# Kernel tuning notes

Measured on AMD Instinct MI355X. Metric: run time of the kernel, lower is better.

Reference implementation:

```python
import jax, jax.numpy as jnp
import numpy as np

ATOM_DIMS = [119, 9, 11, 12, 9, 5, 8, 2, 2]   # torch_geometric smiles x_map cardinalities
EDGE_DIMS = [22, 6, 2]                          # e_map cardinalities
N_NODES = 100_000
N_EDGES = 1_600_000
N_GRAPHS = 1024
HID = 64
MLP_HID = 128
N_LAYERS = 3
BN_EPS = 1e-5


def setup_inputs() -> dict:
    key = jax.random.key(0)
    ks = iter(jax.random.split(key, 64))

    # integer inputs (per-column in-range categorical indices)
    x = jnp.stack([jax.random.randint(next(ks), (N_NODES,), 0, d) for d in ATOM_DIMS], axis=1).astype(jnp.int32)
    edge_attr = jnp.stack([jax.random.randint(next(ks), (N_EDGES,), 0, d) for d in EDGE_DIMS], axis=1).astype(jnp.int32)
    edge_index = jax.random.randint(next(ks), (2, N_EDGES), 0, N_NODES).astype(jnp.int32)
    batch = jnp.sort(jax.random.randint(next(ks), (N_NODES,), 0, N_GRAPHS)).astype(jnp.int32)

    def emb(k, shape, scale=0.1):
        return jax.random.normal(k, shape, dtype=jnp.float32) * scale

    # atom embedding tables, padded to max cardinality and stacked: [9, 119, HID]
    atom_emb = emb(next(ks), (len(ATOM_DIMS), max(ATOM_DIMS), HID))
    # per-layer edge embedding tables: [L, 3, 22, HID]
    edge_emb = emb(next(ks), (N_LAYERS, len(EDGE_DIMS), max(EDGE_DIMS), HID))

    lin1_w = emb(next(ks), (N_LAYERS, MLP_HID, HID))
    lin1_b = emb(next(ks), (N_LAYERS, MLP_HID))
    bn_gamma = 1.0 + emb(next(ks), (N_LAYERS, MLP_HID))
    bn_beta = emb(next(ks), (N_LAYERS, MLP_HID))
    bn_mean = emb(next(ks), (N_LAYERS, MLP_HID))
    bn_var = jax.random.uniform(next(ks), (N_LAYERS, MLP_HID), dtype=jnp.float32, minval=0.5, maxval=1.5)
    lin2_w = emb(next(ks), (N_LAYERS, HID, MLP_HID))
    lin2_b = emb(next(ks), (N_LAYERS, HID))
    eps = jnp.zeros((N_LAYERS,), dtype=jnp.float32)

    return dict(x=x, edge_index=edge_index, edge_attr=edge_attr, batch=batch,
                atom_emb=atom_emb, edge_emb=edge_emb,
                lin1_w=lin1_w, lin1_b=lin1_b, bn_gamma=bn_gamma, bn_beta=bn_beta,
                bn_mean=bn_mean, bn_var=bn_var, lin2_w=lin2_w, lin2_b=lin2_b, eps=eps)


def _feature_embed(tables, idx):
    # tables: [F, V, D], idx: [N, F] -> sum_f tables[f][idx[:, f]] : [N, D]
    return jax.vmap(lambda t, i: t[i], in_axes=(0, 1))(tables, idx).sum(axis=0)


def reference(x, edge_index, edge_attr, batch, atom_emb, edge_emb,
              lin1_w, lin1_b, bn_gamma, bn_beta, bn_mean, bn_var,
              lin2_w, lin2_b, eps):
    n_nodes = x.shape[0]
    src, dst = edge_index[0], edge_index[1]

    h = _feature_embed(atom_emb, x)  # [N, HID]
    pooled = [jax.ops.segment_sum(h, batch, num_segments=N_GRAPHS)]

    for l in range(N_LAYERS):
        e = _feature_embed(edge_emb[l], edge_attr)           # [E, HID]
        msg = jax.nn.relu(h[src] + e)                         # gather + edge embed + relu
        agg = jax.ops.segment_sum(msg, dst, num_segments=n_nodes)  # scatter-add
        z = jax.nn.relu((1.0 + eps[l]) * h + agg)
        # NodeMLP: lin1 -> BatchNorm1d (eval, running stats) -> relu -> lin2
        z = z @ lin1_w[l].T + lin1_b[l]
        z = (z - bn_mean[l]) * jax.lax.rsqrt(bn_var[l] + BN_EPS) * bn_gamma[l] + bn_beta[l]
        z = jax.nn.relu(z)
        h = z @ lin2_w[l].T + lin2_b[l]
        h = jax.nn.relu(h)  # outer relu in GIN.forward (dropout is no-op in eval)
        pooled.append(jax.ops.segment_sum(h, batch, num_segments=N_GRAPHS))

    return jnp.concatenate(pooled, axis=1)  # [G, HID*(L+1)] = [1024, 256]
```

## Files before the change

### kernel.cpp

```cpp
#include <hip/hip_runtime.h>

#define N_NODES 100000
#define N_EDGES 1600000
#define N_GRAPHS 1024
#define HID 64
#define MLP_HID 128
#define N_COMBO 264
#define NBUCK 98
#define BCAP 20480
#define CHUNK 6144

#define NB_EMBED 1563
#define NPREP (3*N_COMBO*HID + 3*MLP_HID*HID + 3*MLP_HID)
#define NB_PREP 296

typedef __attribute__((ext_vector_type(8))) short bf16x8;
typedef __attribute__((ext_vector_type(4))) float f32x4;
typedef __attribute__((ext_vector_type(2))) float f32x2;

static __device__ __forceinline__ float bf2f(unsigned short u) {
    union { unsigned int i; float f; } v; v.i = ((unsigned int)u) << 16; return v.f;
}
static __device__ __forceinline__ unsigned short f2bf(float f) {
    union { float f; unsigned int i; } v; v.f = f;
    unsigned int u = v.i;
    unsigned int r = u + 0x7FFFu + ((u >> 16) & 1u);
    return (unsigned short)(r >> 16);
}
static __device__ __forceinline__ f32x2 bfpair(unsigned int u) {
    union { unsigned int i; float f; } lo, hi;
    lo.i = u << 16;
    hi.i = u & 0xFFFF0000u;
    f32x2 r; r.x = lo.f; r.y = hi.f; return r;
}
static __device__ __forceinline__ unsigned int pack2bf(float a, float b) {
    return (unsigned int)f2bf(a) | ((unsigned int)f2bf(b) << 16);
}

__global__ __launch_bounds__(256) void misc_kernel(
    const int* __restrict__ x, const float* __restrict__ atom_emb,
    const int* __restrict__ batch, unsigned short* __restrict__ h,
    float* __restrict__ out,
    const float* __restrict__ edge_emb,
    const float* __restrict__ w1, const float* __restrict__ w2,
    const float* __restrict__ b1, const float* __restrict__ bn_g,
    const float* __restrict__ bn_b, const float* __restrict__ bn_m,
    const float* __restrict__ bn_v,
    float* __restrict__ comb,
    unsigned short* __restrict__ w1b, unsigned short* __restrict__ w2b,
    float* __restrict__ alpha, float* __restrict__ beta)
{
    const int bid = blockIdx.x;
    const int tid = threadIdx.x;

    if (bid < NB_EMBED) {
        int f = tid & 63;
        int q = __builtin_amdgcn_readfirstlane(tid >> 6);
        int base = bid * 64 + q * 16;
        float run = 0.f;
        int cg = -1;
        for (int k = 0; k < 16; ++k) {
            int gn = base + k;
            if (gn >= N_NODES) break;
            const int* xp = x + gn * 9;
            float acc = 0.f;
#pragma unroll
            for (int j = 0; j < 9; ++j) {
                int idx = xp[j];
                acc += atom_emb[(j * 119 + idx) * HID + f];
            }
            h[(size_t)gn * HID + f] = f2bf(acc);
            int g = batch[gn];
            if (g != cg) {
                if (cg >= 0) atomicAdd(&out[cg * 256 + f], run);
                run = 0.f; cg = g;
            }
            run += acc;
        }
        if (cg >= 0) atomicAdd(&out[cg * 256 + f], run);
    } else {
        int t = (bid - NB_EMBED) * 256 + tid;
        const int NC = 3 * N_COMBO * HID;
        const int NW = 3 * MLP_HID * HID;
        if (t < NC) {
            int d = t & 63;
            int c = (t >> 6) % N_COMBO;
            int l = (t >> 6) / N_COMBO;
            int a0 = c / 12, r = c % 12, a1 = r >> 1, a2 = r & 1;
            const float* base = edge_emb + (size_t)l * 3 * 22 * HID;
            comb[t] = base[(0 * 22 + a0) * HID + d]
                    + base[(1 * 22 + a1) * HID + d]
                    + base[(2 * 22 + a2) * HID + d];
        } else if (t < NC + NW) {
            int i = t - NC;
            w1b[i] = f2bf(w1[i]);
            w2b[i] = f2bf(w2[i]);
        } else if (t < NC + NW + 3 * MLP_HID) {
            int i = t - NC - NW;
            float a = rsqrtf(bn_v[i] + 1e-5f) * bn_g[i];
            alpha[i] = a;
            beta[i] = (b1[i] - bn_m[i]) * a + bn_b[i];
        }
    }
}

__global__ __launch_bounds__(256) void bscatter_kernel(
    const int* __restrict__ ei, const int* __restrict__ ea,
    int* __restrict__ bcur, unsigned long long* __restrict__ ebuf)
{
    __shared__ unsigned long long stage[CHUNK];
    __shared__ int hist[NBUCK];
    __shared__ int lbase[NBUCK];
    __shared__ int shift[NBUCK];
    __shared__ int sbuf[128];

    int tid = threadIdx.x;
    int base = blockIdx.x * CHUNK;
    int n_here = min(CHUNK, N_EDGES - base);

    for (int i = tid; i < NBUCK; i += 256) hist[i] = 0;
    __syncthreads();
    for (int i = tid; i < n_here; i += 256)
        atomicAdd(&hist[ei[N_EDGES + base + i] >> 10], 1);
    __syncthreads();
    if (tid < 128) sbuf[tid] = (tid < NBUCK) ? hist[tid] : 0;
    __syncthreads();
    for (int s = 1; s < 128; s <<= 1) {
        int u = 0;
        if (tid < 128 && tid >= s) u = sbuf[tid - s];
        __syncthreads();
        if (tid < 128) sbuf[tid] += u;
        __syncthreads();
    }
    if (tid < NBUCK) lbase[tid] = sbuf[tid] - hist[tid];
    __syncthreads();
    if (tid < NBUCK) {
        int c = hist[tid];
        if (c > 0) {
            int g = tid * BCAP + atomicAdd(&bcur[tid], c);
            shift[tid] = g - lbase[tid];
        }
        hist[tid] = lbase[tid];
    }
    __syncthreads();
    for (int i = tid; i < n_here; i += 256) {
        int e = base + i;
        int src = ei[e];
        int dst = ei[N_EDGES + e];
        int combo = (ea[e * 3 + 0] * 6 + ea[e * 3 + 1]) * 2 + ea[e * 3 + 2];
        int pos = atomicAdd(&hist[dst >> 10], 1);
        stage[pos] = (unsigned long long)(unsigned)(src | (combo << 17))
                   | ((unsigned long long)(unsigned)dst << 32);
    }
    __syncthreads();
    for (int i = tid; i < n_here; i += 256) {
        unsigned long long en = stage[i];
        ebuf[shift[(int)(en >> 32) >> 10] + i] = en;
    }
}

__global__ __launch_bounds__(256) void csr_build_kernel(
    const unsigned long long* __restrict__ ebuf, const int* __restrict__ bcur,
    int* __restrict__ cnt, int* __restrict__ off, int* __restrict__ csr_e)
{
    __shared__ int nh[1024];
    __shared__ int cur[1024];
    __shared__ int part[256];

    int b = blockIdx.x;
    int tid = threadIdx.x;
    int nodeBase = b << 10;
    int limit = min(1024, N_NODES - nodeBase);
    int beg = b * BCAP;
    int end = beg + bcur[b];

    for (int i = tid; i < 1024; i += 256) nh[i] = 0;
    __syncthreads();
    for (int i = beg + tid; i < end; i += 256)
        atomicAdd(&nh[(int)(ebuf[i] >> 32) - nodeBase], 1);
    __syncthreads();

    int s0 = nh[tid * 4], s1 = nh[tid * 4 + 1], s2 = nh[tid * 4 + 2], s3 = nh[tid * 4 + 3];
    part[tid] = s0 + s1 + s2 + s3;
    __syncthreads();
    for (int st = 1; st < 256; st <<= 1) {
        int v = 0;
        if (tid >= st) v = part[tid - st];
        __syncthreads();
        if (tid >= st) part[tid] += v;
        __syncthreads();
    }
    int e0 = (tid ? part[tid - 1] : 0);
    int e1 = e0 + s0, e2 = e1 + s1, e3 = e2 + s2;
    cur[tid * 4 + 0] = e0; cur[tid * 4 + 1] = e1;
    cur[tid * 4 + 2] = e2; cur[tid * 4 + 3] = e3;
    int excl[4] = {e0, e1, e2, e3};
    int cval[4] = {s0, s1, s2, s3};
#pragma unroll
    for (int j = 0; j < 4; ++j) {
        int nl = tid * 4 + j;
        if (nl < limit) {
            cnt[nodeBase + nl] = cval[j];
            off[nodeBase + nl] = beg + excl[j];
        }
    }
    __syncthreads();
    for (int i = beg + tid; i < end; i += 256) {
        unsigned long long en = ebuf[i];
        int pos = atomicAdd(&cur[(int)(en >> 32) - nodeBase], 1);
        csr_e[beg + pos] = (int)(unsigned)en;
    }
}

__global__ __launch_bounds__(256) void gather_kernel(
    const int* __restrict__ cnt, const int* __restrict__ off,
    const int* __restrict__ csr_e, const unsigned short* __restrict__ h,
    const float* __restrict__ comb_l, const float* __restrict__ eps_p,
    unsigned short* __restrict__ zbuf)
{
    const int tid = threadIdx.x;
    const int lane = tid & 63;
    const int grp = lane >> 3;
    const int fo = (lane & 7) << 3;
    const int n = blockIdx.x * 32 + (tid >> 6) * 8 + grp;

    const int beg = off[n];
    const int end = beg + cnt[n];

    const f32x2 zero2 = {0.f, 0.f};
    f32x2 a0 = zero2, a1 = zero2, a2 = zero2, a3 = zero2;

#define EDGE_ACC(PK)                                                               \
    {                                                                              \
        int pk_ = (PK);                                                            \
        uint4 hv = *reinterpret_cast<const uint4*>(h + (pk_ & 0x1FFFF) * HID + fo);\
        const float4* ep_ = reinterpret_cast<const float4*>(comb_l + (pk_ >> 17) * HID + fo); \
        float4 e0_ = ep_[0], e1_ = ep_[1];                                         \
        a0 += __builtin_elementwise_max(bfpair(hv.x) + (f32x2){e0_.x, e0_.y}, zero2); \
        a1 += __builtin_elementwise_max(bfpair(hv.y) + (f32x2){e0_.z, e0_.w}, zero2); \
        a2 += __builtin_elementwise_max(bfpair(hv.z) + (f32x2){e1_.x, e1_.y}, zero2); \
        a3 += __builtin_elementwise_max(bfpair(hv.w) + (f32x2){e1_.z, e1_.w}, zero2); \
    }

    int i = beg;
    for (; i + 1 < end; i += 2) {
        int pk0 = csr_e[i];
        int pk1 = csr_e[i + 1];
        EDGE_ACC(pk0);
        EDGE_ACC(pk1);
    }
    if (i < end) EDGE_ACC(csr_e[i]);
#undef EDGE_ACC

    uint4 hn = *reinterpret_cast<const uint4*>(h + (size_t)n * HID + fo);
    float ep1 = 1.0f + eps_p[0];
    f32x2 ep2 = {ep1, ep1};
    f32x2 z0 = __builtin_elementwise_max(ep2 * bfpair(hn.x) + a0, zero2);
    f32x2 z1 = __builtin_elementwise_max(ep2 * bfpair(hn.y) + a1, zero2);
    f32x2 z2 = __builtin_elementwise_max(ep2 * bfpair(hn.z) + a2, zero2);
    f32x2 z3 = __builtin_elementwise_max(ep2 * bfpair(hn.w) + a3, zero2);
    uint4 o;
    o.x = pack2bf(z0.x, z0.y);
    o.y = pack2bf(z1.x, z1.y);
    o.z = pack2bf(z2.x, z2.y);
    o.w = pack2bf(z3.x, z3.y);
    *reinterpret_cast<uint4*>(zbuf + (size_t)n * HID + fo) = o;
}

__global__ __launch_bounds__(256) void mlp_kernel(
    const unsigned short* __restrict__ zbuf, unsigned short* __restrict__ h,
    const unsigned short* __restrict__ w1b, const unsigned short* __restrict__ w2b,
    const float* __restrict__ alpha, const float* __restrict__ beta,
    const float* __restrict__ b2, const int* __restrict__ batch,
    float* __restrict__ out, int out_col, int write_h)
{
    __shared__ unsigned short us[128 * MLP_HID];
    __shared__ int sbatch[128];

    const int tid = threadIdx.x;
    const int lane = tid & 63;
    const int w = __builtin_amdgcn_readfirstlane(tid >> 6);
    const int base = blockIdx.x * 128;
    const int r16 = lane & 15;
    const int g4 = lane >> 4;

    if (tid < 128) sbatch[tid] = (base + tid < N_NODES) ? batch[base + tid] : -1;

    bf16x8 awf[2][2];
#pragma unroll
    for (int mo = 0; mo < 2; ++mo)
#pragma unroll
        for (int kt = 0; kt < 2; ++kt) {
            int o = (2 * w + mo) * 16 + r16;
            awf[mo][kt] = *reinterpret_cast<const bf16x8*>(w1b + o * HID + kt * 32 + g4 * 8);
        }
    float4 al[2], be[2];
#pragma unroll
    for (int mo = 0; mo < 2; ++mo) {
        int o0 = (2 * w + mo) * 16 + g4 * 4;
        al[mo] = *reinterpret_cast<const float4*>(alpha + o0);
        be[mo] = *reinterpret_cast<const float4*>(beta + o0);
    }

    char* usb = (char*)us;
#pragma unroll
    for (int nt = 0; nt < 8; ++nt) {
        bf16x8 zf[2];
#pragma unroll
        for (int kt = 0; kt < 2; ++kt)
            zf[kt] = *reinterpret_cast<const bf16x8*>(
                zbuf + (size_t)(base + nt * 16 + r16) * HID + kt * 32 + g4 * 8);
        f32x4 acc[2] = {(f32x4){0.f, 0.f, 0.f, 0.f}, (f32x4){0.f, 0.f, 0.f, 0.f}};
#pragma unroll
        for (int mo = 0; mo < 2; ++mo)
#pragma unroll
            for (int kt = 0; kt < 2; ++kt)
                acc[mo] = __builtin_amdgcn_mfma_f32_16x16x32_bf16(
                    awf[mo][kt], zf[kt], acc[mo], 0, 0, 0);
        int node = nt * 16 + r16;
#pragma unroll
        for (int mo = 0; mo < 2; ++mo) {
            int o0 = (2 * w + mo) * 16 + g4 * 4;
            f32x4 a = acc[mo];
            unsigned lo = pack2bf(fmaxf(a[0] * al[mo].x + be[mo].x, 0.f),
                                  fmaxf(a[1] * al[mo].y + be[mo].y, 0.f));
            unsigned hi = pack2bf(fmaxf(a[2] * al[mo].z + be[mo].z, 0.f),
                                  fmaxf(a[3] * al[mo].w + be[mo].w, 0.f));
            int byte = (node * 256 + o0 * 2) ^ ((node & 7) << 4);
            *reinterpret_cast<uint2*>(usb + byte) = make_uint2(lo, hi);
        }
    }
    __syncthreads();

    bf16x8 b2frag[4];
#pragma unroll
    for (int kt = 0; kt < 4; ++kt)
        b2frag[kt] = *reinterpret_cast<const bf16x8*>(
            w2b + (w * 16 + r16) * MLP_HID + kt * 32 + g4 * 8);

    const int o = w * 16 + r16;
    const float bias = b2[o];
    int gprev = -2;
    float run = 0.f;
#pragma unroll
    for (int mt = 0; mt < 8; ++mt) {
        f32x4 acc2 = (f32x4){0.f, 0.f, 0.f, 0.f};
#pragma unroll
        for (int kt = 0; kt < 4; ++kt) {
            int node = mt * 16 + r16;
            int byte = (node * 256 + (kt * 32 + g4 * 8) * 2) ^ ((node & 7) << 4);
            bf16x8 af = *reinterpret_cast<const bf16x8*>(usb + byte);
            acc2 = __builtin_amdgcn_mfma_f32_16x16x32_bf16(af, b2frag[kt], acc2, 0, 0, 0);
        }
#pragma unroll
        for (int r = 0; r < 4; ++r) {
            int node = mt * 16 + g4 * 4 + r;
            int gn = base + node;
            float v = fmaxf(acc2[r] + bias, 0.f);
            if (write_h && gn < N_NODES) h[(size_t)gn * HID + o] = f2bf(v);
            int gb = sbatch[node];
            if (gb != gprev) {
                if (gprev >= 0) atomicAdd(&out[gprev * 256 + out_col + o], run);
                run = 0.f;
                gprev = gb;
            }
            if (gb >= 0) run += v;
        }
    }
    if (gprev >= 0) atomicAdd(&out[gprev * 256 + out_col + o], run);
}

extern "C" void kernel_launch(void* const* d_in, const int* in_sizes, int n_in,
                              void* d_out, int out_size, void* d_ws, size_t ws_size,
                              hipStream_t stream)
{
    const int*   x        = (const int*)d_in[0];
    const int*   ei       = (const int*)d_in[1];
    const int*   ea       = (const int*)d_in[2];
    const int*   batch    = (const int*)d_in[3];
    const float* atom_emb = (const float*)d_in[4];
    const float* edge_emb = (const float*)d_in[5];
    const float* w1       = (const float*)d_in[6];
    const float* b1       = (const float*)d_in[7];
    const float* bn_g     = (const float*)d_in[8];
    const float* bn_b     = (const float*)d_in[9];
    const float* bn_m     = (const float*)d_in[10];
    const float* bn_v     = (const float*)d_in[11];
    const float* w2       = (const float*)d_in[12];
    const float* b2       = (const float*)d_in[13];
    const float* eps      = (const float*)d_in[14];

    float* out = (float*)d_out;

    const size_t NODE_PAD = 100096;
    char* ws = (char*)d_ws;
    unsigned short* h     = (unsigned short*)ws; ws += NODE_PAD * HID * 2;
    unsigned short* zbuf  = (unsigned short*)ws; ws += NODE_PAD * HID * 2;
    float* comb           = (float*)ws;          ws += (size_t)3 * N_COMBO * HID * 4;
    unsigned short* w1b   = (unsigned short*)ws; ws += (size_t)3 * MLP_HID * HID * 2;
    unsigned short* w2b   = (unsigned short*)ws; ws += (size_t)3 * HID * MLP_HID * 2;
    float* alpha          = (float*)ws;          ws += (size_t)3 * MLP_HID * 4;
    float* betab          = (float*)ws;          ws += (size_t)3 * MLP_HID * 4;
    int*   cnt            = (int*)ws;            ws += (size_t)N_NODES * 4;
    int*   off            = (int*)ws;            ws += (size_t)N_NODES * 4;
    int*   bcur           = (int*)ws;            ws += 128 * 4;
    unsigned long long* ebuf = (unsigned long long*)ws; ws += (size_t)NBUCK * BCAP * 8;
    int*   csr_e          = (int*)ws;            ws += (size_t)NBUCK * BCAP * 4;

    const int nblk128 = (N_NODES + 127) / 128;

    hipMemsetAsync(out, 0, (size_t)N_GRAPHS * 256 * sizeof(float), stream);
    hipMemsetAsync(bcur, 0, 128 * sizeof(int), stream);

    misc_kernel<<<NB_EMBED + NB_PREP, 256, 0, stream>>>(
        x, atom_emb, batch, h, out,
        edge_emb, w1, w2, b1, bn_g, bn_b, bn_m, bn_v,
        comb, w1b, w2b, alpha, betab);

    bscatter_kernel<<<(N_EDGES + CHUNK - 1) / CHUNK, 256, 0, stream>>>(ei, ea, bcur, ebuf);
    csr_build_kernel<<<NBUCK, 256, 0, stream>>>(ebuf, bcur, cnt, off, csr_e);

    for (int l = 0; l < 3; ++l) {
        gather_kernel<<<N_NODES / 32, 256, 0, stream>>>(
            cnt, off, csr_e, h, comb + (size_t)l * N_COMBO * HID, eps + l, zbuf);
        mlp_kernel<<<nblk128, 256, 0, stream>>>(
            zbuf, h,
            w1b + (size_t)l * MLP_HID * HID, w2b + (size_t)l * HID * MLP_HID,
            alpha + (size_t)l * MLP_HID, betab + (size_t)l * MLP_HID,
            b2 + (size_t)l * HID, batch, out, (l + 1) * HID, (l < 2) ? 1 : 0);
    }
}
```

Baseline: 278.1 us.

## Fuse edge gather and node MLP into one per-layer kernel via LDS

Merges the gather/aggregate kernel and the MLP kernel into a single layer kernel. Each 128-node block first aggregates neighbour messages into a swizzled LDS tile, then runs the MFMA MLP on it directly. This drops the zbuf global round trip and one launch per layer. Because the MLP now reads h from other nodes, h is double-buffered so in-place writes cannot race with neighbour reads. The trade-off is fewer gather threads in flight per node, since each thread now handles 4 nodes serially, plus more LDS per block, which can lower occupancy for the latency-bound gather phase.

```diff
diff --git a/kernel.cpp b/kernel.cpp
--- a/kernel.cpp
+++ b/kernel.cpp
@@ -212,28 +212,46 @@
     }
 }
 
-__global__ __launch_bounds__(256) void gather_kernel(
+__global__ __launch_bounds__(256) void layer_kernel(
     const int* __restrict__ cnt, const int* __restrict__ off,
-    const int* __restrict__ csr_e, const unsigned short* __restrict__ h,
+    const int* __restrict__ csr_e, const unsigned short* __restrict__ h_in,
+    unsigned short* __restrict__ h_out,
     const float* __restrict__ comb_l, const float* __restrict__ eps_p,
-    unsigned short* __restrict__ zbuf)
+    const unsigned short* __restrict__ w1b, const unsigned short* __restrict__ w2b,
+    const float* __restrict__ alpha, const float* __restrict__ beta,
+    const float* __restrict__ b2, const int* __restrict__ batch,
+    float* __restrict__ out, int out_col, int write_h)
 {
+    __shared__ unsigned short zs[128 * HID];
+    __shared__ unsigned short us[128 * MLP_HID];
+    __shared__ int sbatch[128];
+
     const int tid = threadIdx.x;
     const int lane = tid & 63;
-    const int grp = lane >> 3;
-    const int fo = (lane & 7) << 3;
-    const int n = blockIdx.x * 32 + (tid >> 6) * 8 + grp;
-
-    const int beg = off[n];
-    const int end = beg + cnt[n];
-
-    const f32x2 zero2 = {0.f, 0.f};
-    f32x2 a0 = zero2, a1 = zero2, a2 = zero2, a3 = zero2;
-
+    const int base = blockIdx.x * 128;
+
+    if (tid < 128) sbatch[tid] = (base + tid < N_NODES) ? batch[base + tid] : -1;
+
+    {
+        const int gg = tid >> 3;
+        const int fo = (tid & 7) << 3;
+        const float ep1 = 1.0f + eps_p[0];
+        const f32x2 ep2 = {ep1, ep1};
+        const f32x2 zero2 = {0.f, 0.f};
+        char* zsb = (char*)zs;
+
+        for (int s = 0; s < 4; ++s) {
+            int node = gg * 4 + s;
+            int n = base + node;
+            uint4 o = make_uint4(0u, 0u, 0u, 0u);
+            if (n < N_NODES) {
+                f32x2 a0 = zero2, a1 = zero2, a2 = zero2, a3 = zero2;
+                int beg = off[n];
+                int end = beg + cnt[n];
 #define EDGE_ACC(PK)                                                               \
     {                                                                              \
         int pk_ = (PK);                                                            \
-        uint4 hv = *reinterpret_cast<const uint4*>(h + (pk_ & 0x1FFFF) * HID + fo);\
+        uint4 hv = *reinterpret_cast<const uint4*>(h_in + (pk_ & 0x1FFFF) * HID + fo);\
         const float4* ep_ = reinterpret_cast<const float4*>(comb_l + (pk_ >> 17) * HID + fo); \
         float4 e0_ = ep_[0], e1_ = ep_[1];                                         \
         a0 += __builtin_elementwise_max(bfpair(hv.x) + (f32x2){e0_.x, e0_.y}, zero2); \
@@ -241,50 +259,36 @@
         a2 += __builtin_elementwise_max(bfpair(hv.z) + (f32x2){e1_.x, e1_.y}, zero2); \
         a3 += __builtin_elementwise_max(bfpair(hv.w) + (f32x2){e1_.z, e1_.w}, zero2); \
     }
-
-    int i = beg;
-    for (; i + 1 < end; i += 2) {
-        int pk0 = csr_e[i];
-        int pk1 = csr_e[i + 1];
-        EDGE_ACC(pk0);
-        EDGE_ACC(pk1);
-    }
-    if (i < end) EDGE_ACC(csr_e[i]);
+                int i = beg;
+                for (; i + 1 < end; i += 2) {
+                    int pk0 = csr_e[i];
+                    int pk1 = csr_e[i + 1];
+                    EDGE_ACC(pk0);
+                    EDGE_ACC(pk1);
+                }
+                if (i < end) EDGE_ACC(csr_e[i]);
 #undef EDGE_ACC
-
-    uint4 hn = *reinterpret_cast<const uint4*>(h + (size_t)n * HID + fo);
-    float ep1 = 1.0f + eps_p[0];
-    f32x2 ep2 = {ep1, ep1};
-    f32x2 z0 = __builtin_elementwise_max(ep2 * bfpair(hn.x) + a0, zero2);
-    f32x2 z1 = __builtin_elementwise_max(ep2 * bfpair(hn.y) + a1, zero2);
-    f32x2 z2 = __builtin_elementwise_max(ep2 * bfpair(hn.z) + a2, zero2);
-    f32x2 z3 = __builtin_elementwise_max(ep2 * bfpair(hn.w) + a3, zero2);
-    uint4 o;
-    o.x = pack2bf(z0.x, z0.y);
-    o.y = pack2bf(z1.x, z1.y);
-    o.z = pack2bf(z2.x, z2.y);
-    o.w = pack2bf(z3.x, z3.y);
-    *reinterpret_cast<uint4*>(zbuf + (size_t)n * HID + fo) = o;
-}
-
-__global__ __launch_bounds__(256) void mlp_kernel(
-    const unsigned short* __restrict__ zbuf, unsigned short* __restrict__ h,
-    const unsigned short* __restrict__ w1b, const unsigned short* __restrict__ w2b,
-    const float* __restrict__ alpha, const float* __restrict__ beta,
-    const float* __restrict__ b2, const int* __restrict__ batch,
-    float* __restrict__ out, int out_col, int write_h)
-{
-    __shared__ unsigned short us[128 * MLP_HID];
-    __shared__ int sbatch[128];
-
-    const int tid = threadIdx.x;
-    const int lane = tid & 63;
+                uint4 hn = *reinterpret_cast<const uint4*>(h_in + (size_t)n * HID + fo);
+                f32x2 z0 = __builtin_elementwise_max(ep2 * bfpair(hn.x) + a0, zero2);
+                f32x2 z1 = __builtin_elementwise_max(ep2 * bfpair(hn.y) + a1, zero2);
+                f32x2 z2 = __builtin_elementwise_max(ep2 * bfpair(hn.z) + a2, zero2);
+                f32x2 z3 = __builtin_elementwise_max(ep2 * bfpair(hn.w) + a3, zero2);
+                o.x = pack2bf(z0.x, z0.y);
+                o.y = pack2bf(z1.x, z1.y);
+                o.z = pack2bf(z2.x, z2.y);
+                o.w = pack2bf(z3.x, z3.y);
+            }
+            int byte = (node * 128 + fo * 2) ^ ((node & 7) << 4);
+            *reinterpret_cast<uint4*>(zsb + byte) = o;
+        }
+    }
+    __syncthreads();
+
     const int w = __builtin_amdgcn_readfirstlane(tid >> 6);
-    const int base = blockIdx.x * 128;
     const int r16 = lane & 15;
     const int g4 = lane >> 4;
-
-    if (tid < 128) sbatch[tid] = (base + tid < N_NODES) ? batch[base + tid] : -1;
+    char* zsb = (char*)zs;
+    char* usb = (char*)us;
 
     bf16x8 awf[2][2];
 #pragma unroll
@@ -302,14 +306,15 @@
         be[mo] = *reinterpret_cast<const float4*>(beta + o0);
     }
 
-    char* usb = (char*)us;
 #pragma unroll
     for (int nt = 0; nt < 8; ++nt) {
+        int node = nt * 16 + r16;
         bf16x8 zf[2];
 #pragma unroll
-        for (int kt = 0; kt < 2; ++kt)
-            zf[kt] = *reinterpret_cast<const bf16x8*>(
-                zbuf + (size_t)(base + nt * 16 + r16) * HID + kt * 32 + g4 * 8);
+        for (int kt = 0; kt < 2; ++kt) {
+            int byte = (node * 128 + (kt * 32 + g4 * 8) * 2) ^ ((node & 7) << 4);
+            zf[kt] = *reinterpret_cast<const bf16x8*>(zsb + byte);
+        }
         f32x4 acc[2] = {(f32x4){0.f, 0.f, 0.f, 0.f}, (f32x4){0.f, 0.f, 0.f, 0.f}};
 #pragma unroll
         for (int mo = 0; mo < 2; ++mo)
@@ -317,7 +322,6 @@
             for (int kt = 0; kt < 2; ++kt)
                 acc[mo] = __builtin_amdgcn_mfma_f32_16x16x32_bf16(
                     awf[mo][kt], zf[kt], acc[mo], 0, 0, 0);
-        int node = nt * 16 + r16;
 #pragma unroll
         for (int mo = 0; mo < 2; ++mo) {
             int o0 = (2 * w + mo) * 16 + g4 * 4;
@@ -357,7 +361,7 @@
             int node = mt * 16 + g4 * 4 + r;
             int gn = base + node;
             float v = fmaxf(acc2[r] + bias, 0.f);
-            if (write_h && gn < N_NODES) h[(size_t)gn * HID + o] = f2bf(v);
+            if (write_h && gn < N_NODES) h_out[(size_t)gn * HID + o] = f2bf(v);
             int gb = sbatch[node];
             if (gb != gprev) {
                 if (gprev >= 0) atomicAdd(&out[gprev * 256 + out_col + o], run);
@@ -394,8 +398,8 @@
 
     const size_t NODE_PAD = 100096;
     char* ws = (char*)d_ws;
-    unsigned short* h     = (unsigned short*)ws; ws += NODE_PAD * HID * 2;
-    unsigned short* zbuf  = (unsigned short*)ws; ws += NODE_PAD * HID * 2;
+    unsigned short* h0    = (unsigned short*)ws; ws += NODE_PAD * HID * 2;
+    unsigned short* h1    = (unsigned short*)ws; ws += NODE_PAD * HID * 2;
     float* comb           = (float*)ws;          ws += (size_t)3 * N_COMBO * HID * 4;
     unsigned short* w1b   = (unsigned short*)ws; ws += (size_t)3 * MLP_HID * HID * 2;
     unsigned short* w2b   = (unsigned short*)ws; ws += (size_t)3 * HID * MLP_HID * 2;
@@ -413,18 +417,18 @@
     hipMemsetAsync(bcur, 0, 128 * sizeof(int), stream);
 
     misc_kernel<<<NB_EMBED + NB_PREP, 256, 0, stream>>>(
-        x, atom_emb, batch, h, out,
+        x, atom_emb, batch, h0, out,
         edge_emb, w1, w2, b1, bn_g, bn_b, bn_m, bn_v,
         comb, w1b, w2b, alpha, betab);
 
     bscatter_kernel<<<(N_EDGES + CHUNK - 1) / CHUNK, 256, 0, stream>>>(ei, ea, bcur, ebuf);
     csr_build_kernel<<<NBUCK, 256, 0, stream>>>(ebuf, bcur, cnt, off, csr_e);
 
+    unsigned short* hbuf[2] = {h0, h1};
     for (int l = 0; l < 3; ++l) {
-        gather_kernel<<<N_NODES / 32, 256, 0, stream>>>(
-            cnt, off, csr_e, h, comb + (size_t)l * N_COMBO * HID, eps + l, zbuf);
-        mlp_kernel<<<nblk128, 256, 0, stream>>>(
-            zbuf, h,
+        layer_kernel<<<nblk128, 256, 0, stream>>>(
+            cnt, off, csr_e, hbuf[l & 1], hbuf[(l & 1) ^ 1],
+            comb + (size_t)l * N_COMBO * HID, eps + l,
             w1b + (size_t)l * MLP_HID * HID, w2b + (size_t)l * HID * MLP_HID,
             alpha + (size_t)l * MLP_HID, betab + (size_t)l * MLP_HID,
             b2 + (size_t)l * HID, batch, out, (l + 1) * HID, (l < 2) ? 1 : 0);
```

Result: slower. 381.1 us (+37.1%).

## Sort nodes by in-degree so gather wavefronts get balanced edge loads

Applied to the files above, without the earlier changes.

Builds an in-degree histogram during CSR construction, scans it, and produces a permutation of nodes grouped by degree. The gather kernel then processes nodes in that order, so the 8 nodes sharing a wavefront have similar edge counts and less divergence or idle lanes. The cost is two extra small kernels with global atomics, plus an indirection that scatters the gather's writes and loses node locality for off/cnt and zbuf.

```diff
diff --git a/kernel.cpp b/kernel.cpp
--- a/kernel.cpp
+++ b/kernel.cpp
@@ -9,6 +9,7 @@
 #define NBUCK 98
 #define BCAP 20480
 #define CHUNK 6144
+#define NDBIN 64
 
 #define NB_EMBED 1563
 #define NPREP (3*N_COMBO*HID + 3*MLP_HID*HID + 3*MLP_HID)
@@ -161,11 +162,13 @@
 
 __global__ __launch_bounds__(256) void csr_build_kernel(
     const unsigned long long* __restrict__ ebuf, const int* __restrict__ bcur,
-    int* __restrict__ cnt, int* __restrict__ off, int* __restrict__ csr_e)
+    int* __restrict__ cnt, int* __restrict__ off, int* __restrict__ csr_e,
+    int* __restrict__ dcnt)
 {
     __shared__ int nh[1024];
     __shared__ int cur[1024];
     __shared__ int part[256];
+    __shared__ int dloc[NDBIN];
 
     int b = blockIdx.x;
     int tid = threadIdx.x;
@@ -175,6 +178,7 @@
     int end = beg + bcur[b];
 
     for (int i = tid; i < 1024; i += 256) nh[i] = 0;
+    if (tid < NDBIN) dloc[tid] = 0;
     __syncthreads();
     for (int i = beg + tid; i < end; i += 256)
         atomicAdd(&nh[(int)(ebuf[i] >> 32) - nodeBase], 1);
@@ -202,9 +206,11 @@
         if (nl < limit) {
             cnt[nodeBase + nl] = cval[j];
             off[nodeBase + nl] = beg + excl[j];
-        }
-    }
-    __syncthreads();
+            atomicAdd(&dloc[min(cval[j], NDBIN - 1)], 1);
+        }
+    }
+    __syncthreads();
+    if (tid < NDBIN && dloc[tid]) atomicAdd(&dcnt[tid], dloc[tid]);
     for (int i = beg + tid; i < end; i += 256) {
         unsigned long long en = ebuf[i];
         int pos = atomicAdd(&cur[(int)(en >> 32) - nodeBase], 1);
@@ -212,17 +218,45 @@
     }
 }
 
+__global__ __launch_bounds__(64) void dscan_kernel(
+    const int* __restrict__ dcnt, int* __restrict__ dbase, int* __restrict__ dcur)
+{
+    __shared__ int buf[NDBIN];
+    int t = threadIdx.x;
+    int v = dcnt[t];
+    buf[t] = v;
+    __syncthreads();
+    if (t == 0) {
+        int run = 0;
+        for (int i = 0; i < NDBIN; ++i) { int c = buf[i]; buf[i] = run; run += c; }
+    }
+    __syncthreads();
+    dbase[t] = buf[t];
+    dcur[t] = buf[t];
+}
+
+__global__ __launch_bounds__(256) void dperm_kernel(
+    const int* __restrict__ cnt, int* __restrict__ dcur, int* __restrict__ perm)
+{
+    int n = blockIdx.x * 256 + threadIdx.x;
+    if (n >= N_NODES) return;
+    int bin = min(cnt[n], NDBIN - 1);
+    int pos = atomicAdd(&dcur[bin], 1);
+    perm[pos] = n;
+}
+
 __global__ __launch_bounds__(256) void gather_kernel(
     const int* __restrict__ cnt, const int* __restrict__ off,
     const int* __restrict__ csr_e, const unsigned short* __restrict__ h,
     const float* __restrict__ comb_l, const float* __restrict__ eps_p,
-    unsigned short* __restrict__ zbuf)
+    const int* __restrict__ perm, unsigned short* __restrict__ zbuf)
 {
     const int tid = threadIdx.x;
     const int lane = tid & 63;
     const int grp = lane >> 3;
     const int fo = (lane & 7) << 3;
-    const int n = blockIdx.x * 32 + (tid >> 6) * 8 + grp;
+    const int gidx = blockIdx.x * 32 + (tid >> 6) * 8 + grp;
+    const int n = perm[gidx];
 
     const int beg = off[n];
     const int end = beg + cnt[n];
@@ -403,14 +437,18 @@
     float* betab          = (float*)ws;          ws += (size_t)3 * MLP_HID * 4;
     int*   cnt            = (int*)ws;            ws += (size_t)N_NODES * 4;
     int*   off            = (int*)ws;            ws += (size_t)N_NODES * 4;
+    int*   perm           = (int*)ws;            ws += (size_t)N_NODES * 4;
     int*   bcur           = (int*)ws;            ws += 128 * 4;
+    int*   dcnt           = (int*)ws;            ws += NDBIN * 4;
+    int*   dbase          = (int*)ws;            ws += NDBIN * 4;
+    int*   dcur           = (int*)ws;            ws += NDBIN * 4;
     unsigned long long* ebuf = (unsigned long long*)ws; ws += (size_t)NBUCK * BCAP * 8;
     int*   csr_e          = (int*)ws;            ws += (size_t)NBUCK * BCAP * 4;
 
     const int nblk128 = (N_NODES + 127) / 128;
 
     hipMemsetAsync(out, 0, (size_t)N_GRAPHS * 256 * sizeof(float), stream);
-    hipMemsetAsync(bcur, 0, 128 * sizeof(int), stream);
+    hipMemsetAsync(bcur, 0, (128 + NDBIN) * sizeof(int), stream);
 
     misc_kernel<<<NB_EMBED + NB_PREP, 256, 0, stream>>>(
         x, atom_emb, batch, h, out,
@@ -418,11 +456,13 @@
         comb, w1b, w2b, alpha, betab);
 
     bscatter_kernel<<<(N_EDGES + CHUNK - 1) / CHUNK, 256, 0, stream>>>(ei, ea, bcur, ebuf);
-    csr_build_kernel<<<NBUCK, 256, 0, stream>>>(ebuf, bcur, cnt, off, csr_e);
+    csr_build_kernel<<<NBUCK, 256, 0, stream>>>(ebuf, bcur, cnt, off, csr_e, dcnt);
+    dscan_kernel<<<1, NDBIN, 0, stream>>>(dcnt, dbase, dcur);
+    dperm_kernel<<<(N_NODES + 255) / 256, 256, 0, stream>>>(cnt, dcur, perm);
 
     for (int l = 0; l < 3; ++l) {
         gather_kernel<<<N_NODES / 32, 256, 0, stream>>>(
-            cnt, off, csr_e, h, comb + (size_t)l * N_COMBO * HID, eps + l, zbuf);
+            cnt, off, csr_e, h, comb + (size_t)l * N_COMBO * HID, eps + l, perm, zbuf);
         mlp_kernel<<<nblk128, 256, 0, stream>>>(
             zbuf, h,
             w1b + (size_t)l * MLP_HID * HID, w2b + (size_t)l * HID * MLP_HID,
```

Measured after the change: 550.3 us. +97.9%, slower.
